# Performance work log

Measured on AMD Instinct MI355X. Metric: run time of the kernel, lower is better.

The kernel has to match this reference:

```python
import jax, jax.numpy as jnp
import numpy as np

D_MODEL = 1024
N_HEADS = 16
D_K = D_MODEL // N_HEADS


def setup_inputs() -> dict:
    key = jax.random.key(0)
    ks = jax.random.split(key, 16)
    B, S = 2, 2048
    sc = 1.0 / np.sqrt(D_MODEL)
    inp = {
        "query": jax.random.normal(ks[0], (B, S, D_MODEL), jnp.float32),
        "key": jax.random.normal(ks[1], (B, S, D_MODEL), jnp.float32),
        "value": jax.random.normal(ks[2], (B, S, D_MODEL), jnp.float32),
        "Wq": jax.random.normal(ks[3], (D_MODEL, D_MODEL), jnp.float32) * sc,
        "bq": jnp.zeros((D_MODEL,), jnp.float32),
        "Wk": jax.random.normal(ks[4], (D_MODEL, D_MODEL), jnp.float32) * sc,
        "bk": jnp.zeros((D_MODEL,), jnp.float32),
        "Wv": jax.random.normal(ks[5], (D_MODEL, D_MODEL), jnp.float32) * sc,
        "bv": jnp.zeros((D_MODEL,), jnp.float32),
        "Wo": jax.random.normal(ks[6], (D_MODEL, D_MODEL), jnp.float32) * sc,
        "bo": jnp.zeros((D_MODEL,), jnp.float32),
        "theta": jax.random.normal(ks[7], (N_HEADS,), jnp.float32) * 0.1,
        "gate": jax.random.normal(ks[8], (D_MODEL,), jnp.float32) * 0.1,
    }
    return inp


def reference(query, key, value, Wq, bq, Wk, bk, Wv, bv, Wo, bo, theta, gate):
    B, Sq, D = query.shape
    Sk = key.shape[1]
    # linear projections (torch Linear: x @ W.T + b), split heads -> [B,H,S,d_k]
    Q = (query @ Wq.T + bq).reshape(B, Sq, N_HEADS, D_K).transpose(0, 2, 1, 3)
    K = (key @ Wk.T + bk).reshape(B, Sk, N_HEADS, D_K).transpose(0, 2, 1, 3)
    V = (value @ Wv.T + bv).reshape(B, Sk, N_HEADS, D_K).transpose(0, 2, 1, 3)

    inv_sqrt_dk = 1.0 / jnp.sqrt(jnp.float32(D_K))
    scores = jnp.einsum("bhqd,bhkd->bhqk", Q, K) * inv_sqrt_dk

    # per-head rotation of the first two feature dims of Q
    cos_t = jnp.cos(theta)[None, :, None, None]  # [1,H,1,1]
    sin_t = jnp.sin(theta)[None, :, None, None]
    q_rot = jnp.concatenate(
        [
            cos_t * Q[..., :1] - sin_t * Q[..., 1:2],
            sin_t * Q[..., :1] + cos_t * Q[..., 1:2],
            Q[..., 2:],
        ],
        axis=-1,
    )
    scores_q = jnp.einsum("bhqd,bhkd->bhqk", q_rot, K) * inv_sqrt_dk

    g_scalar = jax.nn.sigmoid(gate.mean())
    scores = g_scalar * scores_q + (1.0 - g_scalar) * scores

    attn = jax.nn.softmax(scores, axis=-1)
    out = jnp.einsum("bhqk,bhkd->bhqd", attn, V)
    out = out.transpose(0, 2, 1, 3).reshape(B, Sq, D)
    return out @ Wo.T + bo
```

## Files before the change

### kernel.cpp

```cpp
#include <hip/hip_runtime.h>


typedef __bf16 bf16;
typedef __attribute__((ext_vector_type(8))) bf16 bf16x8;
typedef __attribute__((ext_vector_type(4))) bf16 bf16x4;
typedef __attribute__((ext_vector_type(2))) bf16 bf16x2;
typedef __attribute__((ext_vector_type(4))) float f32x4;
typedef unsigned int u32;

#define D_MODEL 1024
#define NH 16
#define DKH 64
#define SEQ 2048

#define GLL16(g, l) __builtin_amdgcn_global_load_lds(                      \
    (const __attribute__((address_space(1))) void*)(g),                    \
    (__attribute__((address_space(3))) void*)(l), 16, 0, 0)

static __device__ __forceinline__ f32x4 mfma16(bf16x8 a, bf16x8 b, f32x4 c) {
  return __builtin_amdgcn_mfma_f32_16x16x32_bf16(a, b, c, 0, 0, 0);
}

static __device__ __forceinline__ u32 pk2(float a, float b) {
  bf16x2 v; v[0] = (bf16)a; v[1] = (bf16)b;
  return __builtin_bit_cast(u32, v);
}

static __device__ __forceinline__ float fexp2(float x) {
#if __has_builtin(__builtin_amdgcn_exp2f)
  return __builtin_amdgcn_exp2f(x);
#else
  return exp2f(x);
#endif
}

#define CQK 0.1803368801111244f
#define MSHIFT 12.0f

__global__ __launch_bounds__(256) void prep(const float* __restrict__ query,
                                            const float* __restrict__ key,
                                            const float* __restrict__ value,
                                            const float* __restrict__ Wq,
                                            const float* __restrict__ bq,
                                            const float* __restrict__ Wk,
                                            const float* __restrict__ Wv,
                                            const float* __restrict__ Wo,
                                            const float* __restrict__ gate,
                                            const float* __restrict__ theta,
                                            bf16* __restrict__ Xq,
                                            bf16* __restrict__ Xk,
                                            bf16* __restrict__ Xv,
                                            bf16* __restrict__ Wqp,
                                            bf16* __restrict__ Wkp,
                                            bf16* __restrict__ Wvp,
                                            bf16* __restrict__ Wop,
                                            float* __restrict__ bqp) {
  const int id = blockIdx.x;
  const int tid = threadIdx.x;
  if (id >= 4096) {
    const int rem = id - 4096;
    const int iz = rem >> 12;
    const int ib = rem & 4095;
    const float* s = (iz == 0) ? query : (iz == 1) ? key : value;
    bf16* d = (iz == 0) ? Xq : (iz == 1) ? Xk : Xv;
    const size_t i = (size_t)(ib * 256 + tid) * 4;
    float4 w = *(const float4*)(s + i);
    bf16x4 o; o[0] = (bf16)w.x; o[1] = (bf16)w.y; o[2] = (bf16)w.z; o[3] = (bf16)w.w;
    *(bf16x4*)(d + i) = o;
    return;
  }
  const int wz = id >> 10, wb = id & 1023;
  if (wz != 0) {
    const float* s = (wz == 1) ? Wk : (wz == 2) ? Wv : Wo;
    bf16* dd = (wz == 1) ? Wkp : (wz == 2) ? Wvp : Wop;
    const size_t i = (size_t)(wb * 256 + tid) * 4;
    float4 v = *(const float4*)(s + i);
    bf16x4 o4; o4[0] = (bf16)v.x; o4[1] = (bf16)v.y; o4[2] = (bf16)v.z; o4[3] = (bf16)v.w;
    *(bf16x4*)(dd + i) = o4;
    return;
  }
  __shared__ float red[4];
  float ssum = 0.f;
  for (int i = tid; i < D_MODEL; i += 256) ssum += gate[i];
#pragma unroll
  for (int off = 32; off > 0; off >>= 1) ssum += __shfl_down(ssum, off);
  if ((tid & 63) == 0) red[tid >> 6] = ssum;
  __syncthreads();
  const float g = 1.f / (1.f + __expf(-(red[0] + red[1] + red[2] + red[3]) / 1024.f));

  const int t = wb * 256 + tid;
  const int r = t >> 8;
  const int c0 = (t & 255) * 4;
  const int d = r & 63, h = r >> 6;
  float4 w = *(const float4*)(Wq + (size_t)r * D_MODEL + c0);
  float4 o;
  if (d == 0) {
    const float a = (g * cosf(theta[h]) + (1.f - g)) * CQK;
    const float bb = (g * sinf(theta[h])) * CQK;
    float4 w2 = *(const float4*)(Wq + (size_t)(r + 1) * D_MODEL + c0);
    o.x = a * w.x - bb * w2.x; o.y = a * w.y - bb * w2.y;
    o.z = a * w.z - bb * w2.z; o.w = a * w.w - bb * w2.w;
    if (c0 == 0) bqp[r] = a * bq[r] - bb * bq[r + 1];
  } else if (d == 1) {
    const float a = (g * cosf(theta[h]) + (1.f - g)) * CQK;
    const float bb = (g * sinf(theta[h])) * CQK;
    float4 w2 = *(const float4*)(Wq + (size_t)(r - 1) * D_MODEL + c0);
    o.x = bb * w2.x + a * w.x; o.y = bb * w2.y + a * w.y;
    o.z = bb * w2.z + a * w.z; o.w = bb * w2.w + a * w.w;
    if (c0 == 0) bqp[r] = bb * bq[r - 1] + a * bq[r];
  } else {
    o.x = CQK * w.x; o.y = CQK * w.y;
    o.z = CQK * w.z; o.w = CQK * w.w;
    if (c0 == 0) bqp[r] = CQK * bq[r];
  }
  bf16x4 ov; ov[0] = (bf16)o.x; ov[1] = (bf16)o.y; ov[2] = (bf16)o.z; ov[3] = (bf16)o.w;
  *(bf16x4*)(Wqp + (size_t)r * D_MODEL + c0) = ov;
}

static __device__ __forceinline__ void gemm_bt_main(const bf16* __restrict__ A,
                                                    const bf16* __restrict__ Bt,
                                                    int tm, int tn, int K,
                                                    f32x4 acc[4][4]) {
  __shared__ bf16 lA[8192];
  __shared__ bf16 lB[8192];
  const int tid = threadIdx.x;
  const int lane = tid & 63, wv = tid >> 6;
  const int wm = wv >> 1, wn = wv & 1;
  const int l16 = lane & 15, lg = lane >> 4;

#pragma unroll
  for (int i = 0; i < 4; ++i)
#pragma unroll
    for (int j = 0; j < 4; ++j) acc[i][j] = (f32x4){0.f, 0.f, 0.f, 0.f};

  int offA[4][2], offB[4][2];
#pragma unroll
  for (int f = 0; f < 4; ++f)
#pragma unroll
    for (int kc = 0; kc < 2; ++kc) {
      const int m = wm * 64 + f * 16 + l16;
      offA[f][kc] = m * 64 + (((kc * 4 + lg) ^ (m & 7)) << 3);
      const int n = wn * 64 + f * 16 + l16;
      offB[f][kc] = n * 64 + (((kc * 4 + lg) ^ (n & 7)) << 3);
    }

  const int rowb = tid >> 3, oct = tid & 7;
  const int soct = oct ^ (rowb & 7);
  const bf16* gA[4];
  const bf16* gB[4];
#pragma unroll
  for (int rd = 0; rd < 4; ++rd) {
    gA[rd] = A + (size_t)(tm + rd * 32 + rowb) * K + soct * 8;
    gB[rd] = Bt + (size_t)(tn + rd * 32 + rowb) * K + soct * 8;
  }

  for (int kt = 0; kt < K; kt += 64) {
    __syncthreads();
#pragma unroll
    for (int rd = 0; rd < 4; ++rd) {
      GLL16(gA[rd] + kt, &lA[rd * 2048 + wv * 512]);
      GLL16(gB[rd] + kt, &lB[rd * 2048 + wv * 512]);
    }
    __syncthreads();
#pragma unroll
    for (int kc = 0; kc < 2; ++kc) {
      bf16x8 af[4], bv[4];
#pragma unroll
      for (int f = 0; f < 4; ++f) {
        af[f] = *(const bf16x8*)&lA[offA[f][kc]];
        bv[f] = *(const bf16x8*)&lB[offB[f][kc]];
      }
#pragma unroll
      for (int i = 0; i < 4; ++i)
#pragma unroll
        for (int j = 0; j < 4; ++j)
          acc[i][j] = mfma16(af[i], bv[j], acc[i][j]);
    }
  }
}

__global__ __launch_bounds__(256) void gemm_qkv(
    const bf16* __restrict__ Xq, const bf16* __restrict__ Xk, const bf16* __restrict__ Xv,
    const bf16* __restrict__ Wq, const bf16* __restrict__ Wk, const bf16* __restrict__ Wv,
    const float* __restrict__ bqp, const float* __restrict__ bk, const float* __restrict__ bv,
    bf16* __restrict__ Qp, bf16* __restrict__ Kp, bf16* __restrict__ Vt) {
  const int wgp = (blockIdx.x & 7) * 96 + (blockIdx.x >> 3);
  const int z = wgp >> 8;
  const int rem = wgp & 255;
  const int tm = (rem >> 3) * 128, tn = (rem & 7) * 128;
  const bf16* A = (z == 0) ? Xq : (z == 1) ? Xk : Xv;
  const bf16* Bt = (z == 0) ? Wq : (z == 1) ? Wk : Wv;
  const float* bias = (z == 0) ? bqp : (z == 1) ? bk : bv;
  f32x4 acc[4][4];
  gemm_bt_main(A, Bt, tm, tn, D_MODEL, acc);
  const int lane = threadIdx.x & 63, wv = threadIdx.x >> 6;
  const int wm = wv >> 1, wn = wv & 1, l16 = lane & 15, lg = lane >> 4;
  if (z < 2) {
    bf16* C = (z == 0) ? Qp : Kp;
#pragma unroll
    for (int i = 0; i < 4; ++i) {
      const int m0 = tm + wm * 64 + i * 16 + lg * 4;
#pragma unroll
      for (int j = 0; j < 4; ++j) {
        const int n = tn + wn * 64 + j * 16 + l16;
        const float bb = bias[n];
        const int h = n >> 6, d = n & 63;
#pragma unroll
        for (int r = 0; r < 4; ++r) {
          const int m = m0 + r;
          const int b = m >> 11, s = m & 2047;
          C[((size_t)(b * NH + h) * SEQ + s) * DKH + d] = (bf16)(acc[i][j][r] + bb);
        }
      }
    }
  } else {
#pragma unroll
    for (int i = 0; i < 4; ++i) {
      const int m0 = tm + wm * 64 + i * 16 + lg * 4;
      const int b = m0 >> 11, s0 = m0 & 2047;
#pragma unroll
      for (int j = 0; j < 4; ++j) {
        const int n = tn + wn * 64 + j * 16 + l16;
        const float bb = bias[n];
        const int h = n >> 6, d = n & 63;
        bf16x4 ov;
#pragma unroll
        for (int r = 0; r < 4; ++r) ov[r] = (bf16)(acc[i][j][r] + bb);
        *(bf16x4*)&Vt[((size_t)(b * NH + h) * DKH + d) * SEQ + s0] = ov;
      }
    }
  }
}

__global__ __launch_bounds__(256) void gemm_out_k(const bf16* __restrict__ A,
                                                  const bf16* __restrict__ Bt,
                                                  const float* __restrict__ bias,
                                                  float* __restrict__ C) {
  const int wgp = (blockIdx.x & 7) * 32 + (blockIdx.x >> 3);
  const int tm = (wgp >> 3) * 128, tn = (wgp & 7) * 128;
  f32x4 acc[4][4];
  gemm_bt_main(A, Bt, tm, tn, D_MODEL, acc);
  const int lane = threadIdx.x & 63, wv = threadIdx.x >> 6;
  const int wm = wv >> 1, wn = wv & 1, l16 = lane & 15, lg = lane >> 4;
#pragma unroll
  for (int i = 0; i < 4; ++i) {
    const int m0 = tm + wm * 64 + i * 16 + lg * 4;
#pragma unroll
    for (int j = 0; j < 4; ++j) {
      const int n = tn + wn * 64 + j * 16 + l16;
      const float bb = bias[n];
#pragma unroll
      for (int r = 0; r < 4; ++r)
        C[(size_t)(m0 + r) * D_MODEL + n] = acc[i][j][r] + bb;
    }
  }
}

__global__ __launch_bounds__(512, 4) void attn_kernel(const bf16* __restrict__ Qp,
                                                      const bf16* __restrict__ Kp,
                                                      const bf16* __restrict__ Vt,
                                                      bf16* __restrict__ Op) {
  __shared__ __align__(16) char smem[49152];
  bf16 (*lK)[4096] = (bf16(*)[4096])smem;
  bf16 (*lV)[4096] = (bf16(*)[4096])(smem + 16384);
  bf16* lP = (bf16*)(smem + 32768);
  float* cmb = (float*)smem;
  float* cl  = (float*)(smem + 32768);

  const int tid = threadIdx.x;
  const int lane = tid & 63, w = tid >> 6;
  const int l16 = lane & 15, lg = lane >> 4;
  const int qg = w >> 1, kg = w & 1;
  const int wgp = (blockIdx.x & 7) * 64 + (blockIdx.x >> 3);
  const int bh = wgp >> 4;
  const int b = bh >> 4, h = bh & 15;
  const int q0 = (wgp & 15) * 128;
  const int qw0 = q0 + qg * 32;
  const size_t kvb = (size_t)bh * SEQ * DKH;

  bf16x8 aq[2][2];
#pragma unroll
  for (int qq = 0; qq < 2; ++qq)
#pragma unroll
    for (int kc = 0; kc < 2; ++kc)
      aq[qq][kc] = *(const bf16x8*)&Qp[kvb +
          (size_t)(qw0 + qq * 16 + l16) * DKH + kc * 32 + lg * 8];

  f32x4 o[2][4];
#pragma unroll
  for (int qq = 0; qq < 2; ++qq)
#pragma unroll
    for (int dt = 0; dt < 4; ++dt) o[qq][dt] = (f32x4){0.f, 0.f, 0.f, 0.f};
  f32x4 lacc[2];
  lacc[0] = (f32x4){0.f, 0.f, 0.f, 0.f};
  lacc[1] = (f32x4){0.f, 0.f, 0.f, 0.f};

  bf16x8 ones;
#pragma unroll
  for (int j = 0; j < 8; ++j) ones[j] = (bf16)1.0f;

  const int kr = tid >> 3, oct = tid & 7;
  const bf16* gK = Kp + kvb + (size_t)kr * DKH + oct * 8;
  const bf16* gV = Vt + kvb + (size_t)kr * SEQ + oct * 8;
  const int swz = kr * 64 + ((oct ^ (kr & 7)) << 3);

  bf16* lPw = &lP[w * 1024];
  int pwr[2][2];
#pragma unroll
  for (int fn = 0; fn < 2; ++fn)
#pragma unroll
    for (int qq = 0; qq < 2; ++qq)
      pwr[fn][qq] = l16 * 64 + (((qq * 4 + fn * 2 + (lg >> 1)) ^ (l16 & 7)) << 3) +
                    ((lg & 1) << 2);
  int prd[2];
#pragma unroll
  for (int qq = 0; qq < 2; ++qq)
    prd[qq] = l16 * 64 + (((qq * 4 + lg) ^ (l16 & 7)) << 3);

  bf16x8 k0r = *(const bf16x8*)(gK);
  bf16x8 v0r = *(const bf16x8*)(gV);
  *(bf16x8*)&lK[0][swz] = k0r;
  *(bf16x8*)&lV[0][swz] = v0r;
  k0r = *(const bf16x8*)(gK + (size_t)64 * DKH);
  v0r = *(const bf16x8*)(gV + 64);
  __syncthreads();

  const int NT = SEQ / 64;
  for (int t = 0; t < NT; ++t) {
    const bf16* K = &lK[t & 1][0];
    const bf16* V = &lV[t & 1][0];

    f32x4 st[2][2];
    __builtin_amdgcn_s_setprio(1);
#pragma unroll
    for (int fn = 0; fn < 2; ++fn) {
      const int row = kg * 32 + fn * 16 + l16;
      bf16x8 ka = *(const bf16x8*)&K[row * 64 + ((lg ^ (row & 7)) << 3)];
      bf16x8 kb = *(const bf16x8*)&K[row * 64 + (((4 + lg) ^ (row & 7)) << 3)];
#pragma unroll
      for (int qq = 0; qq < 2; ++qq) {
        f32x4 tt = (f32x4){0.f, 0.f, 0.f, 0.f};
        tt = mfma16(ka, aq[qq][0], tt);
        tt = mfma16(kb, aq[qq][1], tt);
        st[fn][qq] = tt;
      }
    }
    __builtin_amdgcn_s_setprio(0);

#pragma unroll
    for (int fn = 0; fn < 2; ++fn)
#pragma unroll
      for (int qq = 0; qq < 2; ++qq) {
        uint2 pw;
        pw.x = pk2(fexp2(st[fn][qq][0] - MSHIFT), fexp2(st[fn][qq][1] - MSHIFT));
        pw.y = pk2(fexp2(st[fn][qq][2] - MSHIFT), fexp2(st[fn][qq][3] - MSHIFT));
        *(uint2*)&lPw[pwr[fn][qq]] = pw;
      }

    bf16x8 pa0 = *(const bf16x8*)&lPw[prd[0]];
    bf16x8 pa1 = *(const bf16x8*)&lPw[prd[1]];

    __builtin_amdgcn_s_setprio(1);
    lacc[0] = mfma16(pa0, ones, lacc[0]);
    lacc[1] = mfma16(pa1, ones, lacc[1]);
#pragma unroll
    for (int dt = 0; dt < 4; ++dt) {
      const int n = dt * 16 + l16;
      bf16x8 vv = *(const bf16x8*)&V[n * 64 + (((kg * 4 + lg) ^ (n & 7)) << 3)];
      o[0][dt] = mfma16(pa0, vv, o[0][dt]);
      o[1][dt] = mfma16(pa1, vv, o[1][dt]);
    }
    __builtin_amdgcn_s_setprio(0);

    if (t + 1 < NT) {
      const int nb = (t + 1) & 1;
      *(bf16x8*)&lK[nb][swz] = k0r;
      *(bf16x8*)&lV[nb][swz] = v0r;
      if (t + 2 < NT) {
        const int kt2 = (t + 2) * 64;
        k0r = *(const bf16x8*)(gK + (size_t)kt2 * DKH);
        v0r = *(const bf16x8*)(gV + kt2);
      }
    }
    __syncthreads();
  }

  if (kg == 1) {
#pragma unroll
    for (int qq = 0; qq < 2; ++qq)
#pragma unroll
      for (int dt = 0; dt < 4; ++dt)
        *(f32x4*)&cmb[(size_t)qg * 2048 + ((qq * 4 + dt) * 16 + l16) * 16 + lg * 4] =
            o[qq][dt];
    if (l16 == 0) {
#pragma unroll
      for (int qq = 0; qq < 2; ++qq)
#pragma unroll
        for (int r = 0; r < 4; ++r)
          cl[(qg * 2 + qq) * 16 + lg * 4 + r] = lacc[qq][r];
    }
  }
  __syncthreads();
  if (kg == 0) {
#pragma unroll
    for (int qq = 0; qq < 2; ++qq) {
#pragma unroll
      for (int dt = 0; dt < 4; ++dt) {
        f32x4 p = *(const f32x4*)&cmb[(size_t)qg * 2048 +
                                      ((qq * 4 + dt) * 16 + l16) * 16 + lg * 4];
        o[qq][dt][0] += p[0]; o[qq][dt][1] += p[1];
        o[qq][dt][2] += p[2]; o[qq][dt][3] += p[3];
      }
      float linv[4];
#pragma unroll
      for (int r = 0; r < 4; ++r)
        linv[r] = 1.f / (lacc[qq][r] + cl[(qg * 2 + qq) * 16 + lg * 4 + r]);
#pragma unroll
      for (int r = 0; r < 4; ++r) {
        const int q = qw0 + qq * 16 + lg * 4 + r;
#pragma unroll
        for (int dt = 0; dt < 4; ++dt) {
          const int d = dt * 16 + l16;
          Op[((size_t)(b * SEQ + q)) * D_MODEL + h * DKH + d] =
              (bf16)(o[qq][dt][r] * linv[r]);
        }
      }
    }
  }
}

extern "C" void kernel_launch(void* const* d_in, const int* in_sizes, int n_in,
                              void* d_out, int out_size, void* d_ws, size_t ws_size,
                              hipStream_t stream) {
  (void)in_sizes; (void)n_in; (void)out_size; (void)ws_size;
  const float* query = (const float*)d_in[0];
  const float* key   = (const float*)d_in[1];
  const float* value = (const float*)d_in[2];
  const float* Wq    = (const float*)d_in[3];
  const float* bq    = (const float*)d_in[4];
  const float* Wk    = (const float*)d_in[5];
  const float* bk    = (const float*)d_in[6];
  const float* Wv    = (const float*)d_in[7];
  const float* bv    = (const float*)d_in[8];
  const float* Wo    = (const float*)d_in[9];
  const float* bo    = (const float*)d_in[10];
  const float* theta = (const float*)d_in[11];
  const float* gate  = (const float*)d_in[12];

  float* bqp = (float*)d_ws;
  bf16* wb = (bf16*)((char*)d_ws + 8192);
  bf16* Xq  = wb;
  bf16* Xk  = Xq + 4194304;
  bf16* Xv  = Xk + 4194304;
  bf16* Wqp = Xv + 4194304;
  bf16* Wkp = Wqp + 1048576;
  bf16* Wvp = Wkp + 1048576;
  bf16* Wop = Wvp + 1048576;
  bf16* Qp  = Wop + 1048576;
  bf16* Kp  = Qp + 4194304;
  bf16* Vt  = Kp + 4194304;
  bf16* Op  = Vt + 4194304;

  prep<<<16384, 256, 0, stream>>>(query, key, value, Wq, bq, Wk, Wv, Wo,
                                  gate, theta, Xq, Xk, Xv,
                                  Wqp, Wkp, Wvp, Wop, bqp);
  gemm_qkv<<<768, 256, 0, stream>>>(Xq, Xk, Xv, Wqp, Wkp, Wvp,
                                    bqp, bk, bv, Qp, Kp, Vt);
  attn_kernel<<<512, 512, 0, stream>>>(Qp, Kp, Vt, Op);
  gemm_out_k<<<256, 256, 0, stream>>>(Op, Wop, bo, (float*)d_out);
}
```

Measured before the change: 121.7 us.

## Fuse fp32-to-bf16 input cast into QKV GEMM and enlarge attention KV tiles

The separate prep pass that cast query/key/value to bf16 is removed. The QKV GEMM now loads fp32 activations directly, converts them in registers and writes them to LDS, which saves a full write and re-read of the activations. Separately, the attention kernel's KV tile grows from 64 to 128 keys per iteration with double-buffered LDS (80KB), which halves the number of barriers and loop iterations. The risk is lower occupancy from the larger LDS footprint, and the fp32 A-load path no longer uses async global-to-LDS loads.

Result: slower. 126.5 us (+3.9%).

```diff
diff --git a/kernel.cpp b/kernel.cpp
--- a/kernel.cpp
+++ b/kernel.cpp
@@ -37,19 +37,13 @@
 #define CQK 0.1803368801111244f
 #define MSHIFT 12.0f
 
-__global__ __launch_bounds__(256) void prep(const float* __restrict__ query,
-                                            const float* __restrict__ key,
-                                            const float* __restrict__ value,
-                                            const float* __restrict__ Wq,
+__global__ __launch_bounds__(256) void prep(const float* __restrict__ Wq,
                                             const float* __restrict__ bq,
                                             const float* __restrict__ Wk,
                                             const float* __restrict__ Wv,
                                             const float* __restrict__ Wo,
                                             const float* __restrict__ gate,
                                             const float* __restrict__ theta,
-                                            bf16* __restrict__ Xq,
-                                            bf16* __restrict__ Xk,
-                                            bf16* __restrict__ Xv,
                                             bf16* __restrict__ Wqp,
                                             bf16* __restrict__ Wkp,
                                             bf16* __restrict__ Wvp,
@@ -57,18 +51,6 @@
                                             float* __restrict__ bqp) {
   const int id = blockIdx.x;
   const int tid = threadIdx.x;
-  if (id >= 4096) {
-    const int rem = id - 4096;
-    const int iz = rem >> 12;
-    const int ib = rem & 4095;
-    const float* s = (iz == 0) ? query : (iz == 1) ? key : value;
-    bf16* d = (iz == 0) ? Xq : (iz == 1) ? Xk : Xv;
-    const size_t i = (size_t)(ib * 256 + tid) * 4;
-    float4 w = *(const float4*)(s + i);
-    bf16x4 o; o[0] = (bf16)w.x; o[1] = (bf16)w.y; o[2] = (bf16)w.z; o[3] = (bf16)w.w;
-    *(bf16x4*)(d + i) = o;
-    return;
-  }
   const int wz = id >> 10, wb = id & 1023;
   if (wz != 0) {
     const float* s = (wz == 1) ? Wk : (wz == 2) ? Wv : Wo;
@@ -117,6 +99,81 @@
   *(bf16x4*)(Wqp + (size_t)r * D_MODEL + c0) = ov;
 }
 
+static __device__ __forceinline__ void gemm_f32a_main(const float* __restrict__ A,
+                                                      const bf16* __restrict__ Bt,
+                                                      int tm, int tn, int K,
+                                                      f32x4 acc[4][4]) {
+  __shared__ bf16 lA[8192];
+  __shared__ bf16 lB[8192];
+  const int tid = threadIdx.x;
+  const int lane = tid & 63, wv = tid >> 6;
+  const int wm = wv >> 1, wn = wv & 1;
+  const int l16 = lane & 15, lg = lane >> 4;
+
+#pragma unroll
+  for (int i = 0; i < 4; ++i)
+#pragma unroll
+    for (int j = 0; j < 4; ++j) acc[i][j] = (f32x4){0.f, 0.f, 0.f, 0.f};
+
+  int offA[4][2], offB[4][2];
+#pragma unroll
+  for (int f = 0; f < 4; ++f)
+#pragma unroll
+    for (int kc = 0; kc < 2; ++kc) {
+      const int m = wm * 64 + f * 16 + l16;
+      offA[f][kc] = m * 64 + (((kc * 4 + lg) ^ (m & 7)) << 3);
+      const int n = wn * 64 + f * 16 + l16;
+      offB[f][kc] = n * 64 + (((kc * 4 + lg) ^ (n & 7)) << 3);
+    }
+
+  const int rowb = tid >> 3, oct = tid & 7;
+  const int soct = oct ^ (rowb & 7);
+  const float* gA[4];
+  const bf16* gB[4];
+#pragma unroll
+  for (int rd = 0; rd < 4; ++rd) {
+    gA[rd] = A + (size_t)(tm + rd * 32 + rowb) * K + soct * 8;
+    gB[rd] = Bt + (size_t)(tn + rd * 32 + rowb) * K + soct * 8;
+  }
+
+  for (int kt = 0; kt < K; kt += 64) {
+    __syncthreads();
+#pragma unroll
+    for (int rd = 0; rd < 4; ++rd)
+      GLL16(gB[rd] + kt, &lB[rd * 2048 + wv * 512]);
+    float4 a0[4], a1[4];
+#pragma unroll
+    for (int rd = 0; rd < 4; ++rd) {
+      a0[rd] = *(const float4*)(gA[rd] + kt);
+      a1[rd] = *(const float4*)(gA[rd] + kt + 4);
+    }
+#pragma unroll
+    for (int rd = 0; rd < 4; ++rd) {
+      bf16x8 v;
+      v[0] = (bf16)a0[rd].x; v[1] = (bf16)a0[rd].y;
+      v[2] = (bf16)a0[rd].z; v[3] = (bf16)a0[rd].w;
+      v[4] = (bf16)a1[rd].x; v[5] = (bf16)a1[rd].y;
+      v[6] = (bf16)a1[rd].z; v[7] = (bf16)a1[rd].w;
+      *(bf16x8*)&lA[rd * 2048 + tid * 8] = v;
+    }
+    __syncthreads();
+#pragma unroll
+    for (int kc = 0; kc < 2; ++kc) {
+      bf16x8 af[4], bv[4];
+#pragma unroll
+      for (int f = 0; f < 4; ++f) {
+        af[f] = *(const bf16x8*)&lA[offA[f][kc]];
+        bv[f] = *(const bf16x8*)&lB[offB[f][kc]];
+      }
+#pragma unroll
+      for (int i = 0; i < 4; ++i)
+#pragma unroll
+        for (int j = 0; j < 4; ++j)
+          acc[i][j] = mfma16(af[i], bv[j], acc[i][j]);
+    }
+  }
+}
+
 static __device__ __forceinline__ void gemm_bt_main(const bf16* __restrict__ A,
                                                     const bf16* __restrict__ Bt,
                                                     int tm, int tn, int K,
@@ -180,7 +237,7 @@
 }
 
 __global__ __launch_bounds__(256) void gemm_qkv(
-    const bf16* __restrict__ Xq, const bf16* __restrict__ Xk, const bf16* __restrict__ Xv,
+    const float* __restrict__ Xq, const float* __restrict__ Xk, const float* __restrict__ Xv,
     const bf16* __restrict__ Wq, const bf16* __restrict__ Wk, const bf16* __restrict__ Wv,
     const float* __restrict__ bqp, const float* __restrict__ bk, const float* __restrict__ bv,
     bf16* __restrict__ Qp, bf16* __restrict__ Kp, bf16* __restrict__ Vt) {
@@ -188,11 +245,11 @@
   const int z = wgp >> 8;
   const int rem = wgp & 255;
   const int tm = (rem >> 3) * 128, tn = (rem & 7) * 128;
-  const bf16* A = (z == 0) ? Xq : (z == 1) ? Xk : Xv;
+  const float* A = (z == 0) ? Xq : (z == 1) ? Xk : Xv;
   const bf16* Bt = (z == 0) ? Wq : (z == 1) ? Wk : Wv;
   const float* bias = (z == 0) ? bqp : (z == 1) ? bk : bv;
   f32x4 acc[4][4];
-  gemm_bt_main(A, Bt, tm, tn, D_MODEL, acc);
+  gemm_f32a_main(A, Bt, tm, tn, D_MODEL, acc);
   const int lane = threadIdx.x & 63, wv = threadIdx.x >> 6;
   const int wm = wv >> 1, wn = wv & 1, l16 = lane & 15, lg = lane >> 4;
   if (z < 2) {
@@ -260,12 +317,12 @@
                                                       const bf16* __restrict__ Kp,
                                                       const bf16* __restrict__ Vt,
                                                       bf16* __restrict__ Op) {
-  __shared__ __align__(16) char smem[49152];
-  bf16 (*lK)[4096] = (bf16(*)[4096])smem;
-  bf16 (*lV)[4096] = (bf16(*)[4096])(smem + 16384);
-  bf16* lP = (bf16*)(smem + 32768);
+  __shared__ __align__(16) char smem[81920];
+  bf16 (*lK)[8192] = (bf16(*)[8192])smem;
+  bf16 (*lV)[8192] = (bf16(*)[8192])(smem + 32768);
+  bf16* lP = (bf16*)(smem + 65536);
   float* cmb = (float*)smem;
-  float* cl  = (float*)(smem + 32768);
+  float* cl  = (float*)(smem + 65536);
 
   const int tid = threadIdx.x;
   const int lane = tid & 63, w = tid >> 6;
@@ -300,9 +357,13 @@
   for (int j = 0; j < 8; ++j) ones[j] = (bf16)1.0f;
 
   const int kr = tid >> 3, oct = tid & 7;
-  const bf16* gK = Kp + kvb + (size_t)kr * DKH + oct * 8;
-  const bf16* gV = Vt + kvb + (size_t)kr * SEQ + oct * 8;
-  const int swz = kr * 64 + ((oct ^ (kr & 7)) << 3);
+  const bf16* gK = Kp + kvb + (size_t)kr * DKH + (oct ^ (kr & 7)) * 8;
+  const int kswz0 = kr * 64 + (oct << 3);
+  const int kswz1 = (kr + 64) * 64 + (oct << 3);
+  const int vd = tid >> 4, vsc = tid & 15;
+  const bf16* gV = Vt + kvb + (size_t)vd * SEQ + vsc * 8;
+  const int vswz0 = vd * 128 + ((vsc ^ (vd & 7)) << 3);
+  const int vswz1 = (vd + 32) * 128 + ((vsc ^ (vd & 7)) << 3);
 
   bf16* lPw = &lP[w * 1024];
   int pwr[2][2];
@@ -318,68 +379,78 @@
     prd[qq] = l16 * 64 + (((qq * 4 + lg) ^ (l16 & 7)) << 3);
 
   bf16x8 k0r = *(const bf16x8*)(gK);
+  bf16x8 k1r = *(const bf16x8*)(gK + (size_t)64 * DKH);
   bf16x8 v0r = *(const bf16x8*)(gV);
-  *(bf16x8*)&lK[0][swz] = k0r;
-  *(bf16x8*)&lV[0][swz] = v0r;
-  k0r = *(const bf16x8*)(gK + (size_t)64 * DKH);
-  v0r = *(const bf16x8*)(gV + 64);
+  bf16x8 v1r = *(const bf16x8*)(gV + (size_t)32 * SEQ);
+  *(bf16x8*)&lK[0][kswz0] = k0r;  *(bf16x8*)&lK[0][kswz1] = k1r;
+  *(bf16x8*)&lV[0][vswz0] = v0r;  *(bf16x8*)&lV[0][vswz1] = v1r;
+  k0r = *(const bf16x8*)(gK + (size_t)128 * DKH);
+  k1r = *(const bf16x8*)(gK + (size_t)192 * DKH);
+  v0r = *(const bf16x8*)(gV + 128);
+  v1r = *(const bf16x8*)(gV + (size_t)32 * SEQ + 128);
   __syncthreads();
 
-  const int NT = SEQ / 64;
+  const int NT = SEQ / 128;
   for (int t = 0; t < NT; ++t) {
     const bf16* K = &lK[t & 1][0];
     const bf16* V = &lV[t & 1][0];
 
-    f32x4 st[2][2];
-    __builtin_amdgcn_s_setprio(1);
-#pragma unroll
-    for (int fn = 0; fn < 2; ++fn) {
-      const int row = kg * 32 + fn * 16 + l16;
-      bf16x8 ka = *(const bf16x8*)&K[row * 64 + ((lg ^ (row & 7)) << 3)];
-      bf16x8 kb = *(const bf16x8*)&K[row * 64 + (((4 + lg) ^ (row & 7)) << 3)];
-#pragma unroll
-      for (int qq = 0; qq < 2; ++qq) {
-        f32x4 tt = (f32x4){0.f, 0.f, 0.f, 0.f};
-        tt = mfma16(ka, aq[qq][0], tt);
-        tt = mfma16(kb, aq[qq][1], tt);
-        st[fn][qq] = tt;
-      }
-    }
-    __builtin_amdgcn_s_setprio(0);
-
-#pragma unroll
-    for (int fn = 0; fn < 2; ++fn)
-#pragma unroll
-      for (int qq = 0; qq < 2; ++qq) {
-        uint2 pw;
-        pw.x = pk2(fexp2(st[fn][qq][0] - MSHIFT), fexp2(st[fn][qq][1] - MSHIFT));
-        pw.y = pk2(fexp2(st[fn][qq][2] - MSHIFT), fexp2(st[fn][qq][3] - MSHIFT));
-        *(uint2*)&lPw[pwr[fn][qq]] = pw;
-      }
-
-    bf16x8 pa0 = *(const bf16x8*)&lPw[prd[0]];
-    bf16x8 pa1 = *(const bf16x8*)&lPw[prd[1]];
-
-    __builtin_amdgcn_s_setprio(1);
-    lacc[0] = mfma16(pa0, ones, lacc[0]);
-    lacc[1] = mfma16(pa1, ones, lacc[1]);
-#pragma unroll
-    for (int dt = 0; dt < 4; ++dt) {
-      const int n = dt * 16 + l16;
-      bf16x8 vv = *(const bf16x8*)&V[n * 64 + (((kg * 4 + lg) ^ (n & 7)) << 3)];
-      o[0][dt] = mfma16(pa0, vv, o[0][dt]);
-      o[1][dt] = mfma16(pa1, vv, o[1][dt]);
-    }
-    __builtin_amdgcn_s_setprio(0);
+#pragma unroll
+    for (int ss = 0; ss < 2; ++ss) {
+      f32x4 st[2][2];
+      __builtin_amdgcn_s_setprio(1);
+#pragma unroll
+      for (int fn = 0; fn < 2; ++fn) {
+        const int row = ss * 64 + kg * 32 + fn * 16 + l16;
+        bf16x8 ka = *(const bf16x8*)&K[row * 64 + ((lg ^ (row & 7)) << 3)];
+        bf16x8 kb = *(const bf16x8*)&K[row * 64 + (((4 + lg) ^ (row & 7)) << 3)];
+#pragma unroll
+        for (int qq = 0; qq < 2; ++qq) {
+          f32x4 tt = (f32x4){0.f, 0.f, 0.f, 0.f};
+          tt = mfma16(ka, aq[qq][0], tt);
+          tt = mfma16(kb, aq[qq][1], tt);
+          st[fn][qq] = tt;
+        }
+      }
+      __builtin_amdgcn_s_setprio(0);
+
+#pragma unroll
+      for (int fn = 0; fn < 2; ++fn)
+#pragma unroll
+        for (int qq = 0; qq < 2; ++qq) {
+          uint2 pw;
+          pw.x = pk2(fexp2(st[fn][qq][0] - MSHIFT), fexp2(st[fn][qq][1] - MSHIFT));
+          pw.y = pk2(fexp2(st[fn][qq][2] - MSHIFT), fexp2(st[fn][qq][3] - MSHIFT));
+          *(uint2*)&lPw[pwr[fn][qq]] = pw;
+        }
+
+      bf16x8 pa0 = *(const bf16x8*)&lPw[prd[0]];
+      bf16x8 pa1 = *(const bf16x8*)&lPw[prd[1]];
+
+      __builtin_amdgcn_s_setprio(1);
+      lacc[0] = mfma16(pa0, ones, lacc[0]);
+      lacc[1] = mfma16(pa1, ones, lacc[1]);
+#pragma unroll
+      for (int dt = 0; dt < 4; ++dt) {
+        const int n = dt * 16 + l16;
+        bf16x8 vv = *(const bf16x8*)&V[n * 128 +
+                                      (((ss * 8 + kg * 4 + lg) ^ (n & 7)) << 3)];
+        o[0][dt] = mfma16(pa0, vv, o[0][dt]);
+        o[1][dt] = mfma16(pa1, vv, o[1][dt]);
+      }
+      __builtin_amdgcn_s_setprio(0);
+    }
 
     if (t + 1 < NT) {
       const int nb = (t + 1) & 1;
-      *(bf16x8*)&lK[nb][swz] = k0r;
-      *(bf16x8*)&lV[nb][swz] = v0r;
+      *(bf16x8*)&lK[nb][kswz0] = k0r;  *(bf16x8*)&lK[nb][kswz1] = k1r;
+      *(bf16x8*)&lV[nb][vswz0] = v0r;  *(bf16x8*)&lV[nb][vswz1] = v1r;
       if (t + 2 < NT) {
-        const int kt2 = (t + 2) * 64;
+        const int kt2 = (t + 2) * 128;
         k0r = *(const bf16x8*)(gK + (size_t)kt2 * DKH);
+        k1r = *(const bf16x8*)(gK + (size_t)(kt2 + 64) * DKH);
         v0r = *(const bf16x8*)(gV + kt2);
+        v1r = *(const bf16x8*)(gV + (size_t)32 * SEQ + kt2);
       }
     }
     __syncthreads();
@@ -449,10 +520,7 @@
 
   float* bqp = (float*)d_ws;
   bf16* wb = (bf16*)((char*)d_ws + 8192);
-  bf16* Xq  = wb;
-  bf16* Xk  = Xq + 4194304;
-  bf16* Xv  = Xk + 4194304;
-  bf16* Wqp = Xv + 4194304;
+  bf16* Wqp = wb;
   bf16* Wkp = Wqp + 1048576;
   bf16* Wvp = Wkp + 1048576;
   bf16* Wop = Wvp + 1048576;
@@ -461,10 +529,9 @@
   bf16* Vt  = Kp + 4194304;
   bf16* Op  = Vt + 4194304;
 
-  prep<<<16384, 256, 0, stream>>>(query, key, value, Wq, bq, Wk, Wv, Wo,
-                                  gate, theta, Xq, Xk, Xv,
-                                  Wqp, Wkp, Wvp, Wop, bqp);
-  gemm_qkv<<<768, 256, 0, stream>>>(Xq, Xk, Xv, Wqp, Wkp, Wvp,
+  prep<<<4096, 256, 0, stream>>>(Wq, bq, Wk, Wv, Wo, gate, theta,
+                                 Wqp, Wkp, Wvp, Wop, bqp);
+  gemm_qkv<<<768, 256, 0, stream>>>(query, key, value, Wqp, Wkp, Wvp,
                                     bqp, bk, bv, Qp, Kp, Vt);
   attn_kernel<<<512, 512, 0, stream>>>(Qp, Kp, Vt, Op);
   gemm_out_k<<<256, 256, 0, stream>>>(Op, Wop, bo, (float*)d_out);
```
